# Performance work log

Measured on AMD Instinct MI355X. Metric: run time of the kernel, lower is better.

Reference implementation:

```python
import jax, jax.numpy as jnp
import numpy as np

S, D, H, HD, FF = 4096, 1024, 16, 64, 4096  # seq, d_embed, heads, head_dim, hidden
EPS = 1e-6  # flax LayerNorm default epsilon


def layer_norm(x, scale, bias):
    mu = jnp.mean(x, axis=-1, keepdims=True)
    var = jnp.var(x, axis=-1, keepdims=True)
    return (x - mu) * jax.lax.rsqrt(var + EPS) * scale + bias


def rope(x):
    # x: [S, H, HD]; standard half-split rotary embedding, base 10000
    half = x.shape[-1] // 2
    freq = 1.0 / (10000.0 ** (jnp.arange(half, dtype=x.dtype) / half))  # [half]
    ang = jnp.arange(x.shape[0], dtype=x.dtype)[:, None] * freq          # [S, half]
    cos = jnp.cos(ang)[:, None, :]
    sin = jnp.sin(ang)[:, None, :]
    x1, x2 = x[..., :half], x[..., half:]
    return jnp.concatenate([x1 * cos - x2 * sin, x2 * cos + x1 * sin], axis=-1)


def setup_inputs() -> dict:
    key = jax.random.key(0)
    ks = jax.random.split(key, 8)
    s = 0.02
    return {
        "x": jax.random.normal(ks[0], (S, D), jnp.float32),
        "ln1_scale": jnp.ones((D,), jnp.float32), "ln1_bias": jnp.zeros((D,), jnp.float32),
        "ln2_scale": jnp.ones((D,), jnp.float32), "ln2_bias": jnp.zeros((D,), jnp.float32),
        "Wq": jax.random.normal(ks[1], (D, H, HD), jnp.float32) * s, "bq": jnp.zeros((H, HD), jnp.float32),
        "Wk": jax.random.normal(ks[2], (D, H, HD), jnp.float32) * s, "bk": jnp.zeros((H, HD), jnp.float32),
        "Wv": jax.random.normal(ks[3], (D, H, HD), jnp.float32) * s, "bv": jnp.zeros((H, HD), jnp.float32),
        "Wo": jax.random.normal(ks[4], (H, HD, D), jnp.float32) * s, "bo": jnp.zeros((D,), jnp.float32),
        "W1": jax.random.normal(ks[5], (D, FF), jnp.float32) * s, "b1": jnp.zeros((FF,), jnp.float32),
        "W2": jax.random.normal(ks[6], (FF, D), jnp.float32) * s, "b2": jnp.zeros((D,), jnp.float32),
    }


def reference(x, ln1_scale, ln1_bias, ln2_scale, ln2_bias, Wq, bq, Wk, bk, Wv, bv, Wo, bo, W1, b1, W2, b2):
    # Pre-LN attention block with RoPE fused into QK scores
    y = layer_norm(x, ln1_scale, ln1_bias)
    q = jnp.einsum('sd,dhc->shc', y, Wq) + bq  # [S,H,HD]
    k = jnp.einsum('sd,dhc->shc', y, Wk) + bk
    v = jnp.einsum('sd,dhc->shc', y, Wv) + bv
    q = rope(q)
    k = rope(k)
    scores = jnp.einsum('qhc,khc->hqk', q, k) / jnp.sqrt(jnp.asarray(HD, x.dtype))  # [H,S,S]
    p = jax.nn.softmax(scores, axis=-1)
    o = jnp.einsum('hqk,khc->qhc', p, v)                # [S,H,HD]
    attn_out = jnp.einsum('qhc,hcd->qd', o, Wo) + bo    # [S,D]
    x = x + attn_out
    # Pre-LN GELU MLP block
    y = layer_norm(x, ln2_scale, ln2_bias)
    y = jax.nn.gelu(y @ W1 + b1, approximate=False)
    x = x + (y @ W2 + b2)
    return x
```

## Files before the change

### kernel.cpp

```cpp
#include <hip/hip_runtime.h>
#include <hip/hip_bf16.h>
#include <math.h>

using bf16 = __hip_bfloat16;
typedef __attribute__((ext_vector_type(8))) short short8;
typedef __attribute__((ext_vector_type(4))) short s16x4;
typedef __attribute__((ext_vector_type(4))) float f32x4;

constexpr int S = 4096, D = 1024, H = 16, HD = 64, FF = 4096;

static __device__ __forceinline__ float tof(bf16 v) { return __bfloat162float(v); }
static __device__ __forceinline__ bf16 tob(float v) { return __float2bfloat16(v); }
static __device__ __forceinline__ short tobs(float v) {
    bf16 h = __float2bfloat16(v);
    return *reinterpret_cast<short*>(&h);
}
static __device__ __forceinline__ unsigned pkbf16(float a, float b) {
    __hip_bfloat162 h = __float22bfloat162_rn(make_float2(a, b));
    return *reinterpret_cast<unsigned*>(&h);
}

#if __has_builtin(__builtin_amdgcn_exp2f)
#define EXP2(x) __builtin_amdgcn_exp2f(x)
#else
#define EXP2(x) exp2f(x)
#endif

static __device__ __forceinline__ f32x4 mfma16(short8 a, short8 b, f32x4 c) {
    return __builtin_amdgcn_mfma_f32_16x16x32_bf16(a, b, c, 0, 0, 0);
}
static __device__ __forceinline__ void stage16(const bf16* g, bf16* l) {
    __builtin_amdgcn_global_load_lds((__attribute__((address_space(1))) void*)g,
                                     (__attribute__((address_space(3))) void*)l, 16, 0, 0);
}

__global__ __launch_bounds__(256) void ln_kernel(const float* __restrict__ x,
                                                 const float* __restrict__ scale,
                                                 const float* __restrict__ bias,
                                                 bf16* __restrict__ y) {
    int row = blockIdx.x, t = threadIdx.x;
    const float* xr = x + (size_t)row * D;
    float v[4], s = 0.f, ss = 0.f;
#pragma unroll
    for (int i = 0; i < 4; ++i) {
        v[i] = xr[t + 256 * i];
        s += v[i]; ss += v[i] * v[i];
    }
    __shared__ float r0[256], r1[256];
    r0[t] = s; r1[t] = ss;
    __syncthreads();
    for (int off = 128; off; off >>= 1) {
        if (t < off) { r0[t] += r0[t + off]; r1[t] += r1[t + off]; }
        __syncthreads();
    }
    float mu  = r0[0] * (1.f / D);
    float var = r1[0] * (1.f / D) - mu * mu;
    float inv = rsqrtf(var + 1e-6f);
    bf16* yr = y + (size_t)row * D;
#pragma unroll
    for (int i = 0; i < 4; ++i) {
        int c = t + 256 * i;
        yr[c] = tob((v[i] - mu) * inv * scale[c] + bias[c]);
    }
}

__global__ __launch_bounds__(256) void wtrans_all(
    const float* __restrict__ Wq, const float* __restrict__ Wk,
    const float* __restrict__ Wv, const float* __restrict__ Wo,
    const float* __restrict__ W1, const float* __restrict__ W2,
    const float* __restrict__ bq, const float* __restrict__ bk,
    const float* __restrict__ bv,
    bf16* __restrict__ BTqkv, bf16* __restrict__ BTo,
    bf16* __restrict__ BT1, bf16* __restrict__ BT2, float* __restrict__ bqkv) {
    int id = blockIdx.x;
    if (id >= 12288) {
        int i = (id - 12288) * 256 + threadIdx.x;
        bqkv[i] = i < 1024 ? bq[i] : (i < 2048 ? bk[i - 1024] : bv[i - 2048]);
        return;
    }
    const float* W; bf16* dst; int K, N, local;
    if (id < 3072)      { int s = id >> 10; W = s == 0 ? Wq : (s == 1 ? Wk : Wv);
                          dst = BTqkv + (size_t)s * 1048576; K = 1024; N = 1024; local = id & 1023; }
    else if (id < 4096) { W = Wo; dst = BTo; K = 1024; N = 1024; local = id - 3072; }
    else if (id < 8192) { W = W1; dst = BT1; K = 1024; N = 4096; local = id - 4096; }
    else                { W = W2; dst = BT2; K = 4096; N = 1024; local = id - 8192; }
    int ls = (N == 4096) ? 7 : 5;
    int nt = (local & ((1 << ls) - 1)) << 5, kt = (local >> ls) << 5;
    __shared__ float t[32][33];
    int tid = threadIdx.x, r = tid >> 5, c = tid & 31;
#pragma unroll
    for (int p = 0; p < 4; ++p)
        t[r + p * 8][c] = W[(size_t)(kt + r + p * 8) * N + nt + c];
    __syncthreads();
#pragma unroll
    for (int p = 0; p < 4; ++p)
        dst[(size_t)(nt + r + p * 8) * K + kt + c] = tob(t[c][r + p * 8]);
}

#define EPI_RES  1
#define EPI_GELU 2
#define EPI_QKV  3
#define EPI_PART 4

template <int EPI, int MT>
__global__ __launch_bounds__(256, MT == 128 ? 2 : 3) void gemm_bt(
    const bf16* __restrict__ A, const bf16* __restrict__ BT,
    const float* __restrict__ bias, const float* resid, void* out, void* out2,
    int M, int N, int K, int kLen) {
    constexpr int NJ = (MT == 128) ? 4 : 2;
    __shared__ bf16 As[MT * 32];
    __shared__ bf16 Bs[128 * 32];
    const int tid = threadIdx.x;
    const int w = tid >> 6, lane = tid & 63;
    const int quad = lane >> 4, l16 = lane & 15;
    const int rowBase = blockIdx.y * MT, colBase = blockIdx.x * 128;
    const int kStart = blockIdx.z * kLen;
    const int wr = (MT == 128) ? (w >> 1) * 64 : 0;
    const int wc = (MT == 128) ? (w & 1) * 64 : w * 32;
    const int sr = lane >> 2, skb = (lane & 3) * 8;
    f32x4 acc[4][NJ] = {};
    for (int k0 = 0; k0 < kLen; k0 += 32) {
        __syncthreads();
        if (MT == 128) {
#pragma unroll
            for (int t = 0; t < 2; ++t) {
                int inst = w * 2 + t;
                int r = inst * 16 + sr;
                stage16(A  + (size_t)(rowBase + r) * K + kStart + k0 + skb, As + inst * 512);
                stage16(BT + (size_t)(colBase + r) * K + kStart + k0 + skb, Bs + inst * 512);
            }
        } else {
            stage16(A + (size_t)(rowBase + w * 16 + sr) * K + kStart + k0 + skb, As + w * 512);
#pragma unroll
            for (int t = 0; t < 2; ++t) {
                int inst = w + t * 4;
                stage16(BT + (size_t)(colBase + inst * 16 + sr) * K + kStart + k0 + skb, Bs + inst * 512);
            }
        }
        __syncthreads();
        const bf16* pa = As + (wr + l16) * 32 + quad * 8;
        const bf16* pb = Bs + (wc + l16) * 32 + quad * 8;
        short8 a[4], b[NJ];
#pragma unroll
        for (int i = 0; i < 4; ++i) a[i] = *(const short8*)(pa + i * 512);
#pragma unroll
        for (int j = 0; j < NJ; ++j) b[j] = *(const short8*)(pb + j * 512);
#pragma unroll
        for (int i = 0; i < 4; ++i)
#pragma unroll
            for (int j = 0; j < NJ; ++j) acc[i][j] = mfma16(a[i], b[j], acc[i][j]);
    }
    if (EPI == EPI_QKV) {
        bf16* QKo = (bf16*)out;
        bf16* VTo = (bf16*)out2;
        if (colBase >= 2048) {
#pragma unroll
            for (int j = 0; j < NJ; ++j) {
                int c = colBase + wc + j * 16 + l16;
                float bj = bias[c];
                size_t cc = (size_t)(c - 2048) * 4096;
#pragma unroll
                for (int i = 0; i < 4; ++i) {
                    int r0 = rowBase + wr + i * 16 + quad * 4;
                    s16x4 ov = {tobs(acc[i][j][0] + bj), tobs(acc[i][j][1] + bj),
                                tobs(acc[i][j][2] + bj), tobs(acc[i][j][3] + bj)};
                    *(s16x4*)(VTo + cc + r0) = ov;
                }
            }
        } else {
            const bool isq = colBase < 1024;
            const float qs = isq ? 0.125f * 1.44269504088896f : 1.f;
#pragma unroll
            for (int j2 = 0; j2 < 2; ++j2) {
                int dim = j2 * 16 + l16;
                float freq = __expf(-(float)dim * (9.210340371976184f / 32.f));
                int c1 = colBase + wc + j2 * 16 + l16, c2 = c1 + 32;
                float b1v = bias[c1], b2v = bias[c2];
#pragma unroll
                for (int i = 0; i < 4; ++i) {
#pragma unroll
                    for (int reg = 0; reg < 4; ++reg) {
                        int s = rowBase + wr + i * 16 + quad * 4 + reg;
                        float sn, cs;
                        sincosf((float)s * freq, &sn, &cs);
                        float x1 = acc[i][j2][reg] + b1v;
                        float x2 = acc[i][j2 + 2][reg] + b2v;
                        QKo[(size_t)s * 2048 + c1] = tob((x1 * cs - x2 * sn) * qs);
                        QKo[(size_t)s * 2048 + c2] = tob((x2 * cs + x1 * sn) * qs);
                    }
                }
            }
        }
    } else {
#pragma unroll
        for (int j = 0; j < NJ; ++j) {
            int c = colBase + wc + j * 16 + l16;
            float bj = (EPI == EPI_PART) ? 0.f : bias[c];
#pragma unroll
            for (int i = 0; i < 4; ++i) {
                int r0 = rowBase + wr + i * 16 + quad * 4;
#pragma unroll
                for (int reg = 0; reg < 4; ++reg) {
                    size_t idx = (size_t)(r0 + reg) * N + c;
                    float val = acc[i][j][reg] + bj;
                    if (EPI == EPI_RES) {
                        ((float*)out)[idx] = val + resid[idx];
                    } else if (EPI == EPI_PART) {
                        ((float*)out)[(size_t)blockIdx.z * M * N + idx] = val;
                    } else {
                        float g = 0.5f * val * (1.f + erff(val * 0.70710678118f));
                        ((bf16*)out)[idx] = tob(g);
                    }
                }
            }
        }
    }
}

__global__ __launch_bounds__(256, 4) void attn_kernel(const bf16* __restrict__ QK,
                                                      const bf16* __restrict__ VT,
                                                      float* __restrict__ Op,
                                                      float* __restrict__ lp) {
    const int bx = blockIdx.x;
    const int h = bx >> 6, qb = (bx & 63) >> 1, kh = bx & 1;
    const int w = threadIdx.x >> 6, lane = threadIdx.x & 63;
    const int quad = lane >> 4, l16 = lane & 15;
    const int q0w = qb * 128 + w * 32;
    const bf16* Qh = QK + h * 64;
    const bf16* Kh = QK + 1024 + h * 64;
    const bf16* Vh = VT + (size_t)h * 64 * 4096;

    __shared__ char smem[32768];
    bf16* Ks = (bf16*)(smem);
    bf16* Vs = (bf16*)(smem + 8192);
    char* Pw = smem + 16384 + w * 4096;

    const int sw = l16 & 7;
    const int rloc = lane >> 3, slot = lane & 7;
    const int schunk = (slot ^ rloc) * 8;
    const int row0 = w * 16 + rloc, row1 = w * 16 + 8 + rloc;

    short8 qf[2][2];
#pragma unroll
    for (int qt = 0; qt < 2; ++qt)
#pragma unroll
        for (int c = 0; c < 2; ++c)
            qf[qt][c] = *(const short8*)(Qh + (size_t)(q0w + qt * 16 + l16) * 2048 + c * 32 + quad * 8);

    const short ob = (l16 == 0) ? (short)0x3F80 : (short)0;
    const short8 ones8 = {ob, ob, ob, ob, ob, ob, ob, ob};

    f32x4 acc[4][2] = {};
    f32x4 accl[2] = {};
    const f32x4 zero = {0.f, 0.f, 0.f, 0.f};
    const int ktBeg = kh * 2048;

    for (int kt = 0; kt < 2048; kt += 64) {
        const int ktA = ktBeg + kt;
        __syncthreads();
        stage16(Kh + (size_t)(ktA + row0) * 2048 + schunk, Ks + w * 1024);
        stage16(Kh + (size_t)(ktA + row1) * 2048 + schunk, Ks + w * 1024 + 512);
        stage16(Vh + (size_t)row0 * 4096 + ktA + schunk, Vs + w * 1024);
        stage16(Vh + (size_t)row1 * 4096 + ktA + schunk, Vs + w * 1024 + 512);
        __syncthreads();

        f32x4 st[4][2];
#pragma unroll
        for (int nt = 0; nt < 4; ++nt) {
            const bf16* kr = Ks + (nt * 16 + l16) * 64;
            short8 k0 = *(const short8*)(kr + ((quad ^ sw) * 8));
            short8 k1 = *(const short8*)(kr + (((quad + 4) ^ sw) * 8));
#pragma unroll
            for (int qt = 0; qt < 2; ++qt)
                st[nt][qt] = mfma16(k1, qf[qt][1], mfma16(k0, qf[qt][0], zero));
        }
#pragma unroll
        for (int nt = 0; nt < 4; ++nt)
#pragma unroll
            for (int qt = 0; qt < 2; ++qt) {
                float e0 = EXP2(st[nt][qt][0]), e1 = EXP2(st[nt][qt][1]);
                float e2 = EXP2(st[nt][qt][2]), e3 = EXP2(st[nt][qt][3]);
                uint2 pk = {pkbf16(e0, e1), pkbf16(e2, e3)};
                *(uint2*)(Pw + (qt * 16 + l16) * 128 +
                          (((nt * 2 + (quad >> 1)) ^ sw) * 16) + (quad & 1) * 8) = pk;
            }
        asm volatile("s_waitcnt lgkmcnt(0)" ::: "memory");
#pragma unroll
        for (int c = 0; c < 2; ++c) {
            short8 pB[2];
#pragma unroll
            for (int qt = 0; qt < 2; ++qt) {
                pB[qt] = *(const short8*)(Pw + (qt * 16 + l16) * 128 + (((c * 4 + quad) ^ sw) * 16));
                accl[qt] = mfma16(ones8, pB[qt], accl[qt]);
            }
#pragma unroll
            for (int vt = 0; vt < 4; ++vt) {
                short8 vf = *(const short8*)(Vs + (vt * 16 + l16) * 64 + (((c * 4 + quad) ^ sw) * 8));
#pragma unroll
                for (int qt = 0; qt < 2; ++qt)
                    acc[vt][qt] = mfma16(vf, pB[qt], acc[vt][qt]);
            }
        }
    }
    float* Oz = Op + (size_t)kh * (4096 * 1024);
#pragma unroll
    for (int qt = 0; qt < 2; ++qt) {
        int q = q0w + qt * 16 + l16;
#pragma unroll
        for (int vt = 0; vt < 4; ++vt)
            *(f32x4*)(Oz + (size_t)q * 1024 + h * 64 + vt * 16 + quad * 4) = acc[vt][qt];
        if (quad == 0) lp[kh * 65536 + h * 4096 + q] = accl[qt][0];
    }
}

__global__ __launch_bounds__(256) void merge_attn(const float* __restrict__ Op,
                                                  const float* __restrict__ lp,
                                                  bf16* __restrict__ o) {
    int i = blockIdx.x * 256 + threadIdx.x;
    int d4 = i * 4;
    int s = d4 >> 10, d = d4 & 1023, h = d >> 6;
    f32x4 a = *(const f32x4*)(Op + d4 + (size_t)s * 0);
    f32x4 b = *(const f32x4*)(Op + 4194304 + d4);
    float linv = 1.f / (lp[h * 4096 + s] + lp[65536 + h * 4096 + s]);
    s16x4 ov = {tobs(a[0] + b[0]) , 0, 0, 0};
    ov[0] = tobs((a[0] + b[0]) * linv);
    ov[1] = tobs((a[1] + b[1]) * linv);
    ov[2] = tobs((a[2] + b[2]) * linv);
    ov[3] = tobs((a[3] + b[3]) * linv);
    *(s16x4*)(o + d4) = ov;
}

__global__ __launch_bounds__(256) void merge_ffn2(const float* __restrict__ pb,
                                                  const float* __restrict__ b2,
                                                  float* __restrict__ out) {
    int i = blockIdx.x * 256 + threadIdx.x;
    int d4 = i * 4, c = d4 & 1023;
    f32x4 a = *(const f32x4*)(pb + d4);
    f32x4 b = *(const f32x4*)(pb + 4194304 + d4);
    f32x4 r = *(const f32x4*)(out + d4);
    f32x4 bb = *(const f32x4*)(b2 + c);
    f32x4 v = {a[0] + b[0] + r[0] + bb[0], a[1] + b[1] + r[1] + bb[1],
               a[2] + b[2] + r[2] + bb[2], a[3] + b[3] + r[3] + bb[3]};
    *(f32x4*)(out + d4) = v;
}

extern "C" void kernel_launch(void* const* d_in, const int* in_sizes, int n_in,
                              void* d_out, int out_size, void* d_ws, size_t ws_size,
                              hipStream_t stream) {
    const float* x   = (const float*)d_in[0];
    const float* s1  = (const float*)d_in[1];
    const float* b1n = (const float*)d_in[2];
    const float* s2  = (const float*)d_in[3];
    const float* b2n = (const float*)d_in[4];
    const float* Wq  = (const float*)d_in[5];
    const float* bq  = (const float*)d_in[6];
    const float* Wk  = (const float*)d_in[7];
    const float* bk  = (const float*)d_in[8];
    const float* Wv  = (const float*)d_in[9];
    const float* bv  = (const float*)d_in[10];
    const float* Wo  = (const float*)d_in[11];
    const float* bo  = (const float*)d_in[12];
    const float* W1  = (const float*)d_in[13];
    const float* b1  = (const float*)d_in[14];
    const float* W2  = (const float*)d_in[15];
    const float* b2  = (const float*)d_in[16];

    char* ws = (char*)d_ws;
    bf16*  y    = (bf16*)(ws);
    bf16*  QK   = (bf16*)(ws + (8ull  << 20));
    bf16*  BTo  = (bf16*)(ws + (24ull << 20));
    float* lp   = (float*)(ws + (26ull << 20));
    float* bqkv = (float*)(ws + (27ull << 20));
    bf16*  o    = (bf16*)(ws + (32ull << 20));
    bf16*  hb   = (bf16*)(ws + (40ull << 20));
    bf16*  BTqkv= (bf16*)(ws + (40ull << 20));
    float* Op   = (float*)(ws + (40ull << 20));
    bf16*  VT   = (bf16*)(ws + (72ull << 20));
    bf16*  BT1  = (bf16*)(ws + (80ull << 20));
    bf16*  BT2  = (bf16*)(ws + (88ull << 20));
    float* pb   = (float*)(ws);
    float* x1   = (float*)d_out;

    wtrans_all<<<12300, 256, 0, stream>>>(Wq, Wk, Wv, Wo, W1, W2, bq, bk, bv,
                                          BTqkv, BTo, BT1, BT2, bqkv);

    ln_kernel<<<S, 256, 0, stream>>>(x, s1, b1n, y);

    gemm_bt<EPI_QKV, 128><<<dim3(24, 32), 256, 0, stream>>>(y, BTqkv, bqkv, nullptr, QK, VT, S, 3072, D, D);

    attn_kernel<<<H * 64, 256, 0, stream>>>(QK, VT, Op, lp);
    merge_attn<<<4096, 256, 0, stream>>>(Op, lp, o);

    gemm_bt<EPI_RES, 64><<<dim3(8, 64), 256, 0, stream>>>(o, BTo, bo, x, x1, nullptr, S, D, D, D);

    ln_kernel<<<S, 256, 0, stream>>>(x1, s2, b2n, y);

    gemm_bt<EPI_GELU, 128><<<dim3(32, 32), 256, 0, stream>>>(y, BT1, b1, nullptr, hb, nullptr, S, FF, D, D);

    gemm_bt<EPI_PART, 64><<<dim3(8, 64, 2), 256, 0, stream>>>(hb, BT2, b2, nullptr, pb, nullptr, S, D, FF, 2048);
    merge_ffn2<<<4096, 256, 0, stream>>>(pb, b2, x1);
}
```

Before: 425.3 us.

## Double-buffer K/V staging and shuffle P in registers via permlane swaps

Splits the attention kernel's LDS into two 16 KB buffers so the next K/V tile is prefetched with global_load_lds while the current tile is computed, using explicit vmcnt waits and raw s_barrier. It also removes the LDS round trip for the softmax probabilities: the exp'd scores are packed to bf16 and rearranged into MFMA B-operand layout with v_permlane32_swap/v_permlane16_swap. The aim is to hide global load latency and cut LDS write/read traffic and the lgkmcnt wait. The risks are the correctness of the permlane shuffle mapping and the hand-written waitcnt/barrier ordering.

```diff
diff --git a/kernel.cpp b/kernel.cpp
--- a/kernel.cpp
+++ b/kernel.cpp
@@ -32,6 +32,12 @@
 static __device__ __forceinline__ void stage16(const bf16* g, bf16* l) {
     __builtin_amdgcn_global_load_lds((__attribute__((address_space(1))) void*)g,
                                      (__attribute__((address_space(3))) void*)l, 16, 0, 0);
+}
+static __device__ __forceinline__ void pl32swap(unsigned& a, unsigned& b) {
+    asm("v_permlane32_swap_b32 %0, %1" : "+v"(a), "+v"(b));
+}
+static __device__ __forceinline__ void pl16swap(unsigned& a, unsigned& b) {
+    asm("v_permlane16_swap_b32 %0, %1" : "+v"(a), "+v"(b));
 }
 
 __global__ __launch_bounds__(256) void ln_kernel(const float* __restrict__ x,
@@ -231,9 +237,6 @@
     const bf16* Vh = VT + (size_t)h * 64 * 4096;
 
     __shared__ char smem[32768];
-    bf16* Ks = (bf16*)(smem);
-    bf16* Vs = (bf16*)(smem + 8192);
-    char* Pw = smem + 16384 + w * 4096;
 
     const int sw = l16 & 7;
     const int rloc = lane >> 3, slot = lane & 7;
@@ -255,42 +258,64 @@
     const f32x4 zero = {0.f, 0.f, 0.f, 0.f};
     const int ktBeg = kh * 2048;
 
-    for (int kt = 0; kt < 2048; kt += 64) {
-        const int ktA = ktBeg + kt;
-        __syncthreads();
-        stage16(Kh + (size_t)(ktA + row0) * 2048 + schunk, Ks + w * 1024);
-        stage16(Kh + (size_t)(ktA + row1) * 2048 + schunk, Ks + w * 1024 + 512);
-        stage16(Vh + (size_t)row0 * 4096 + ktA + schunk, Vs + w * 1024);
-        stage16(Vh + (size_t)row1 * 4096 + ktA + schunk, Vs + w * 1024 + 512);
-        __syncthreads();
-
-        f32x4 st[4][2];
+    {
+        bf16* Ksb = (bf16*)smem;
+        bf16* Vsb = (bf16*)(smem + 8192);
+        stage16(Kh + (size_t)(ktBeg + row0) * 2048 + schunk, Ksb + w * 1024);
+        stage16(Kh + (size_t)(ktBeg + row1) * 2048 + schunk, Ksb + w * 1024 + 512);
+        stage16(Vh + (size_t)row0 * 4096 + ktBeg + schunk, Vsb + w * 1024);
+        stage16(Vh + (size_t)row1 * 4096 + ktBeg + schunk, Vsb + w * 1024 + 512);
+    }
+
+#pragma unroll 2
+    for (int t = 0; t < 32; ++t) {
+        char* curb = smem + (t & 1) * 16384;
+        char* nxtb = smem + ((t + 1) & 1) * 16384;
+        __builtin_amdgcn_s_barrier();
+        if (t < 31) {
+            const int ktA = ktBeg + (t + 1) * 64;
+            bf16* Ksb = (bf16*)nxtb;
+            bf16* Vsb = (bf16*)(nxtb + 8192);
+            stage16(Kh + (size_t)(ktA + row0) * 2048 + schunk, Ksb + w * 1024);
+            stage16(Kh + (size_t)(ktA + row1) * 2048 + schunk, Ksb + w * 1024 + 512);
+            stage16(Vh + (size_t)row0 * 4096 + ktA + schunk, Vsb + w * 1024);
+            stage16(Vh + (size_t)row1 * 4096 + ktA + schunk, Vsb + w * 1024 + 512);
+            asm volatile("s_waitcnt vmcnt(4)" ::: "memory");
+        } else {
+            asm volatile("s_waitcnt vmcnt(0)" ::: "memory");
+        }
+        __builtin_amdgcn_s_barrier();
+
+        const bf16* Ks = (const bf16*)curb;
+        const bf16* Vs = (const bf16*)(curb + 8192);
+
+        unsigned u[4][2][2];
 #pragma unroll
         for (int nt = 0; nt < 4; ++nt) {
             const bf16* kr = Ks + (nt * 16 + l16) * 64;
             short8 k0 = *(const short8*)(kr + ((quad ^ sw) * 8));
             short8 k1 = *(const short8*)(kr + (((quad + 4) ^ sw) * 8));
 #pragma unroll
-            for (int qt = 0; qt < 2; ++qt)
-                st[nt][qt] = mfma16(k1, qf[qt][1], mfma16(k0, qf[qt][0], zero));
-        }
-#pragma unroll
-        for (int nt = 0; nt < 4; ++nt)
-#pragma unroll
             for (int qt = 0; qt < 2; ++qt) {
-                float e0 = EXP2(st[nt][qt][0]), e1 = EXP2(st[nt][qt][1]);
-                float e2 = EXP2(st[nt][qt][2]), e3 = EXP2(st[nt][qt][3]);
-                uint2 pk = {pkbf16(e0, e1), pkbf16(e2, e3)};
-                *(uint2*)(Pw + (qt * 16 + l16) * 128 +
-                          (((nt * 2 + (quad >> 1)) ^ sw) * 16) + (quad & 1) * 8) = pk;
-            }
-        asm volatile("s_waitcnt lgkmcnt(0)" ::: "memory");
+                f32x4 st = mfma16(k1, qf[qt][1], mfma16(k0, qf[qt][0], zero));
+                u[nt][qt][0] = pkbf16(EXP2(st[0]), EXP2(st[1]));
+                u[nt][qt][1] = pkbf16(EXP2(st[2]), EXP2(st[3]));
+            }
+        }
 #pragma unroll
         for (int c = 0; c < 2; ++c) {
             short8 pB[2];
 #pragma unroll
             for (int qt = 0; qt < 2; ++qt) {
-                pB[qt] = *(const short8*)(Pw + (qt * 16 + l16) * 128 + (((c * 4 + quad) ^ sw) * 16));
+                unsigned a0 = u[2 * c][qt][0], a1 = u[2 * c][qt][1];
+                unsigned b0 = u[2 * c + 1][qt][0], b1 = u[2 * c + 1][qt][1];
+                pl32swap(a0, b0);
+                pl32swap(a1, b1);
+                pl16swap(a0, b0);
+                pl16swap(a1, b1);
+                union { unsigned u4[4]; short8 s8; } pk;
+                pk.u4[0] = a0; pk.u4[1] = a1; pk.u4[2] = b0; pk.u4[3] = b1;
+                pB[qt] = pk.s8;
                 accl[qt] = mfma16(ones8, pB[qt], accl[qt]);
             }
 #pragma unroll
```

Result: no change. 429.6 us (+1.0%).
